# Optimization experiments

Measured on AMD Instinct MI355X. Metric: run time of the kernel, lower is better.

The kernel has to match this reference:

```python
import jax, jax.numpy as jnp
import numpy as np

B, S, D = 16, 1024, 384
H, DH = 6, 64  # head_dim = hidden // heads


def setup_inputs() -> dict:
    key = jax.random.key(0)
    ks = jax.random.split(key, 9)
    std = 0.02
    return {
        "x": jax.random.normal(ks[0], (B, S, D), jnp.float32),
        "Wq": jax.random.normal(ks[1], (H, D, DH), jnp.float32) * std,
        "bq": jax.random.normal(ks[2], (H, DH), jnp.float32) * std,
        "Wk": jax.random.normal(ks[3], (H, D, DH), jnp.float32) * std,
        "bk": jax.random.normal(ks[4], (H, DH), jnp.float32) * std,
        "Wv": jax.random.normal(ks[5], (H, D, DH), jnp.float32) * std,
        "bv": jax.random.normal(ks[6], (H, DH), jnp.float32) * std,
        "Wo": jax.random.normal(ks[7], (D, D), jnp.float32) * std,  # [out, in] like nn.Linear
        "bo": jax.random.normal(ks[8], (D,), jnp.float32) * std,
    }


def reference(x, Wq, bq, Wk, bk, Wv, bv, Wo, bo):
    # Per-head q/k/v projections (stacked over heads h)
    q = jnp.einsum("bsd,hde->bhse", x, Wq) + bq[None, :, None, :]
    k = jnp.einsum("bsd,hde->bhse", x, Wk) + bk[None, :, None, :]
    v = jnp.einsum("bsd,hde->bhse", x, Wv) + bv[None, :, None, :]
    # Explicit softmax attention (dropout prob = 0.0 in config)
    scores = jnp.einsum("bhse,bhte->bhst", q, k) / jnp.sqrt(jnp.float32(DH))
    probs = jax.nn.softmax(scores, axis=-1)
    ctx = jnp.einsum("bhst,bhte->bhse", probs, v)  # [B,H,S,DH]
    # Concat heads along last dim: [B,S,H*DH]
    concat = jnp.transpose(ctx, (0, 2, 1, 3)).reshape(B, S, H * DH)
    # Output projection (nn.Linear: y = x @ W^T + b)
    out = jnp.einsum("bsd,ed->bse", concat, Wo) + bo
    return out
```

## Files before the change

### kernel.cpp

```cpp
#include <hip/hip_runtime.h>
#include <hip/hip_bf16.h>

typedef __attribute__((ext_vector_type(8))) short short8;
typedef __attribute__((ext_vector_type(4))) short short4v;
typedef __attribute__((ext_vector_type(4))) float float4v;
typedef __attribute__((ext_vector_type(2))) float float2v;
typedef __attribute__((ext_vector_type(4))) int int4v;

#define MFMA16(a,b,c) __builtin_amdgcn_mfma_f32_16x16x32_bf16((a),(b),(c),0,0,0)
#define EXP2(x) __builtin_amdgcn_exp2f(x)

static constexpr int Bz = 16, Sq = 1024, Dm = 384, Hh = 6, Dh = 64;
static constexpr int Mtok = Bz * Sq;
static constexpr int NQKV = 1152;

__device__ __forceinline__ short f2bf(float f) {
  union { float f; unsigned u; } v; v.f = f;
  unsigned r = v.u + 0x7fffu + ((v.u >> 16) & 1u);
  return (short)(r >> 16);
}

__device__ __forceinline__ unsigned cvtpk(float a, float b) {
  unsigned d;
  asm("v_cvt_pk_bf16_f32 %0, %1, %2" : "=v"(d) : "v"(a), "v"(b));
  return d;
}

__device__ __forceinline__ void gload16(const void* src, void* lds) {
  __builtin_amdgcn_global_load_lds(
      (const __attribute__((address_space(1))) unsigned int*)src,
      (__attribute__((address_space(3))) unsigned int*)lds, 16, 0, 0);
}

__device__ __forceinline__ int vperm(int s) {
  return (s & ~31) | ((s & 12) << 1) | ((s & 16) >> 2) | (s & 3);
}

__global__ __launch_bounds__(256) void conv_x(const float* __restrict__ x,
                                              short* __restrict__ xb) {
  const int i = (blockIdx.x * 256 + threadIdx.x) * 8;
  float4v v0 = *(const float4v*)(x + i);
  float4v v1 = *(const float4v*)(x + i + 4);
  short8 o;
  o[0] = f2bf(v0[0]); o[1] = f2bf(v0[1]); o[2] = f2bf(v0[2]); o[3] = f2bf(v0[3]);
  o[4] = f2bf(v1[0]); o[5] = f2bf(v1[1]); o[6] = f2bf(v1[2]); o[7] = f2bf(v1[3]);
  *(short8*)(xb + i) = o;
}

__global__ __launch_bounds__(256) void conv_w(const float* __restrict__ Wq,
                                              const float* __restrict__ Wk,
                                              const float* __restrict__ Wv,
                                              const float* __restrict__ bq,
                                              const float* __restrict__ bk,
                                              const float* __restrict__ bv,
                                              const float* __restrict__ Wo,
                                              short* __restrict__ Wt,
                                              float* __restrict__ bias,
                                              short* __restrict__ Wob) {
  const float SCL = 0.125f * 1.44269504088896340736f;
  const int i = blockIdx.x * 256 + threadIdx.x;
  const int NW = NQKV * Dm;
  if (i < NW) {
    const int c = i / Dm, d = i % Dm;
    const int p = c / 384, rr = c % 384;
    const int h = rr >> 6, dh = rr & 63;
    const float* W = (p == 0) ? Wq : ((p == 1) ? Wk : Wv);
    float w = W[(h * Dm + d) * Dh + dh];
    if (p == 0) w *= SCL;
    Wt[c * Dm + d] = f2bf(w);
  } else if (i < NW + NQKV) {
    const int c = i - NW;
    const int p = c / 384, rr = c % 384;
    const int h = rr >> 6, dh = rr & 63;
    const float* bb = (p == 0) ? bq : ((p == 1) ? bk : bv);
    float b = bb[h * Dh + dh];
    if (p == 0) b *= SCL;
    bias[c] = b;
  } else if (i < NW + NQKV + Dm * Dm) {
    const int j = i - NW - NQKV;
    Wob[j] = f2bf(Wo[j]);
  }
}

__global__ __launch_bounds__(256) void qkv_gemm(const short* __restrict__ Xb,
                                                const short* __restrict__ Wt,
                                                const float* __restrict__ bias,
                                                short* __restrict__ qkv,
                                                short* __restrict__ vt) {
  __shared__ char smem[49152];
  const int tid = threadIdx.x;
  const int wave = tid >> 6, lane = tid & 63;
  const int r = lane & 15, g = lane >> 4;
  const int wr = wave >> 1, wc = wave & 1;

  const int flat = blockIdx.x;
  const int w = (flat & 7) * 144 + (flat >> 3);
  const int bx = w % 9, by = w / 9;
  const int bm0 = by * 128, bn0 = bx * 128;
  const int m0 = bm0 + wr * 64, n0 = bn0 + wc * 64;

  float bv_n[4];
#pragma unroll
  for (int ni = 0; ni < 4; ++ni) bv_n[ni] = bias[n0 + ni * 16 + r];
  asm volatile("s_waitcnt vmcnt(0)" ::: "memory");

  const char *aSrc0, *aSrc1, *bSrc0, *bSrc1;
  {
    const int o0 = tid * 16, o1 = 4096 + tid * 16;
    const int lr0 = o0 >> 7, cb0 = (o0 & 127) ^ ((lr0 & 7) << 4);
    const int lr1 = o1 >> 7, cb1 = (o1 & 127) ^ ((lr1 & 7) << 4);
    const int m_0 = 2 * lr0 + (cb0 >> 6), kb0 = cb0 & 63;
    const int m_1 = 2 * lr1 + (cb1 >> 6), kb1 = cb1 & 63;
    aSrc0 = (const char*)(Xb + (bm0 + m_0) * Dm) + kb0;
    aSrc1 = (const char*)(Xb + (bm0 + m_1) * Dm) + kb1;
    bSrc0 = (const char*)(Wt + (bn0 + m_0) * Dm) + kb0;
    bSrc1 = (const char*)(Wt + (bn0 + m_1) * Dm) + kb1;
  }
  auto stage = [&](int t, int buf) {
    char* base = smem + buf * 16384;
    const int kb = t * 64;
    gload16(aSrc0 + kb, base + wave * 1024);
    gload16(aSrc1 + kb, base + 4096 + wave * 1024);
    gload16(bSrc0 + kb, base + 8192 + wave * 1024);
    gload16(bSrc1 + kb, base + 12288 + wave * 1024);
  };

  int aOff[4], bOff[4];
#pragma unroll
  for (int i = 0; i < 4; ++i) {
    const int m = wr * 64 + i * 16 + r;
    const int lr = m >> 1;
    aOff[i] = lr * 128 + ((((m & 1) << 6) | (16 * g)) ^ ((lr & 7) << 4));
    const int n = wc * 64 + i * 16 + r;
    const int lrn = n >> 1;
    bOff[i] = 8192 + lrn * 128 + ((((n & 1) << 6) | (16 * g)) ^ ((lrn & 7) << 4));
  }

  float4v acc[4][4] = {};
  auto compute = [&](int buf) {
    const char* sb = smem + buf * 16384;
    short8 a[4], b[4];
#pragma unroll
    for (int i = 0; i < 4; ++i) a[i] = *(const short8*)(sb + aOff[i]);
#pragma unroll
    for (int i = 0; i < 4; ++i) b[i] = *(const short8*)(sb + bOff[i]);
#pragma unroll
    for (int mi = 0; mi < 4; ++mi)
#pragma unroll
      for (int ni = 0; ni < 4; ++ni)
        acc[mi][ni] = MFMA16(a[mi], b[ni], acc[mi][ni]);
  };

  stage(0, 0);
  stage(1, 1);
#pragma unroll 1
  for (int t = 0; t < 10; ++t) {
    asm volatile("s_waitcnt vmcnt(4)" ::: "memory");
    __builtin_amdgcn_s_barrier();
    compute(t % 3);
    stage(t + 2, (t + 2) % 3);
  }
  asm volatile("s_waitcnt vmcnt(4)" ::: "memory");
  __builtin_amdgcn_s_barrier();
  compute(1);
  asm volatile("s_waitcnt vmcnt(0)" ::: "memory");
  __builtin_amdgcn_s_barrier();
  compute(2);

#pragma unroll
  for (int ni = 0; ni < 4; ++ni) {
    const int col = n0 + ni * 16 + r;
    const int p = col / 384, rr2 = col % 384;
    const int h = rr2 >> 6, dh = rr2 & 63;
    const float bv = bv_n[ni];
#pragma unroll
    for (int mi = 0; mi < 4; ++mi) {
#pragma unroll
      for (int rp = 0; rp < 2; ++rp) {
        const unsigned u = cvtpk(acc[mi][ni][2 * rp] + bv,
                                 acc[mi][ni][2 * rp + 1] + bv);
        const int mg = m0 + mi * 16 + 4 * g + 2 * rp;
        if (p < 2) {
          qkv[mg * NQKV + col] = (short)u;
          qkv[(mg + 1) * NQKV + col] = (short)(u >> 16);
        } else {
          const int bb = mg >> 10, s = mg & 1023;
          const int sp = vperm(s);
          short* vp = vt + ((bb * Hh + h) * Dh + dh) * Sq;
          *(unsigned*)(vp + sp) = u;
        }
      }
    }
  }
}

__global__ __launch_bounds__(256) void attn(const short* __restrict__ qkv,
                                            const short* __restrict__ vt,
                                            short* __restrict__ ctx) {
  __shared__ char smem[49152];
  const int tid = threadIdx.x;
  const int wave = tid >> 6, lane = tid & 63;
  const int r = lane & 15, g = lane >> 4;
  const int xr = (r & 7) << 4;
  const int flat = blockIdx.x;
  const int w = (flat & 7) * 96 + (flat >> 3);
  const int qb = w & 7, bh = w >> 3;
  const int b = bh / Hh, h = bh % Hh;
  const int tok0 = b * Sq;
  const int qw = qb * 128 + wave * 32;

  short8 qf[2][2];
#pragma unroll
  for (int f = 0; f < 2; ++f) {
    const short* qp = qkv + (tok0 + qw + 16 * f + r) * NQKV + h * Dh;
    qf[f][0] = *(const short8*)(qp + 8 * g);
    qf[f][1] = *(const short8*)(qp + 32 + 8 * g);
  }
  asm volatile("s_waitcnt vmcnt(0)" ::: "memory");

  const short* kg = qkv + tok0 * NQKV + 384 + h * Dh;
  const short* vg = vt + (b * Hh + h) * Dh * Sq;

  const int o0 = wave * 2048 + lane * 16;
  const int row0 = o0 >> 7, cb0 = (o0 & 127) ^ ((row0 & 7) << 4);
  const int o1 = o0 + 1024;
  const int row1 = o1 >> 7, cb1 = (o1 & 127) ^ ((row1 & 7) << 4);

#define STAGE(T, BUFSEL)                                                        \
  {                                                                             \
    char* kb_ = smem + (BUFSEL) * 16384;                                        \
    const int kv_ = (T) * 64;                                                   \
    gload16((const char*)(kg + (kv_ + row0) * NQKV) + cb0, kb_ + wave * 2048);  \
    gload16((const char*)(vg + row0 * Sq + kv_) + cb0, kb_ + 8192 + wave * 2048);\
    gload16((const char*)(kg + (kv_ + row1) * NQKV) + cb1, kb_ + wave * 2048 + 1024);\
    gload16((const char*)(vg + row1 * Sq + kv_) + cb1, kb_ + 8192 + wave * 2048 + 1024);\
  }

  int kOff[4][2], vOff[4][2];
#pragma unroll
  for (int kt = 0; kt < 4; ++kt)
#pragma unroll
    for (int c = 0; c < 2; ++c)
      kOff[kt][c] = (16 * kt + r) * 128 + ((64 * c + 16 * g) ^ xr);
#pragma unroll
  for (int d = 0; d < 4; ++d)
#pragma unroll
    for (int h2 = 0; h2 < 2; ++h2)
      vOff[d][h2] = (16 * d + r) * 128 + ((64 * h2 + 16 * g) ^ xr);

  float4v acc[4][2] = {};
  float2v lsum2[2] = {};

  auto compute = [&](int bufsel) {
    const char* kb = smem + bufsel * 16384;
    const char* vb = kb + 8192;
    short8 kf[4][2];
#pragma unroll
    for (int kt = 0; kt < 4; ++kt) {
      kf[kt][0] = *(const short8*)(kb + kOff[kt][0]);
      kf[kt][1] = *(const short8*)(kb + kOff[kt][1]);
    }
    short8 vf[4][2];
#pragma unroll
    for (int d = 0; d < 4; ++d)
#pragma unroll
      for (int h2 = 0; h2 < 2; ++h2)
        vf[d][h2] = *(const short8*)(vb + vOff[d][h2]);
    float4v s[4][2];
    __builtin_amdgcn_s_setprio(1);
#pragma unroll
    for (int kt = 0; kt < 4; ++kt)
#pragma unroll
      for (int f = 0; f < 2; ++f) {
        float4v z = {};
        z = MFMA16(kf[kt][0], qf[f][0], z);
        z = MFMA16(kf[kt][1], qf[f][1], z);
        s[kt][f] = z;
      }
    __builtin_amdgcn_s_setprio(0);
    short8 pa[2][2];
#pragma unroll
    for (int f = 0; f < 2; ++f) {
      float2v ps2 = {};
#pragma unroll
      for (int h2 = 0; h2 < 2; ++h2) {
        float e0[4], e1[4];
#pragma unroll
        for (int j = 0; j < 4; ++j) {
          e0[j] = EXP2(s[2 * h2][f][j]);
          e1[j] = EXP2(s[2 * h2 + 1][f][j]);
        }
#pragma unroll
        for (int j = 0; j < 2; ++j) {
          float2v p0 = {e0[2 * j], e0[2 * j + 1]};
          float2v p1 = {e1[2 * j], e1[2 * j + 1]};
          ps2 += p0 + p1;
        }
        int4v wv;
        wv[0] = (int)cvtpk(e0[0], e0[1]);
        wv[1] = (int)cvtpk(e0[2], e0[3]);
        wv[2] = (int)cvtpk(e1[0], e1[1]);
        wv[3] = (int)cvtpk(e1[2], e1[3]);
        pa[f][h2] = __builtin_bit_cast(short8, wv);
      }
      lsum2[f] += ps2;
    }
    __builtin_amdgcn_s_setprio(1);
#pragma unroll
    for (int d = 0; d < 4; ++d)
#pragma unroll
      for (int f = 0; f < 2; ++f) {
        acc[d][f] = MFMA16(pa[f][0], vf[d][0], acc[d][f]);
        acc[d][f] = MFMA16(pa[f][1], vf[d][1], acc[d][f]);
      }
    __builtin_amdgcn_s_setprio(0);
  };

  STAGE(0, 0)
  STAGE(1, 1)
#pragma unroll 1
  for (int t = 0; t < 14; ++t) {
    asm volatile("s_waitcnt vmcnt(4)" ::: "memory");
    __builtin_amdgcn_s_barrier();
    compute(t % 3);
    STAGE(t + 2, (t + 2) % 3)
  }
  asm volatile("s_waitcnt vmcnt(4)" ::: "memory");
  __builtin_amdgcn_s_barrier();
  compute(2);
  asm volatile("s_waitcnt vmcnt(0)" ::: "memory");
  __builtin_amdgcn_s_barrier();
  compute(0);

#pragma unroll
  for (int f = 0; f < 2; ++f) {
    float lsum = lsum2[f][0] + lsum2[f][1];
    lsum += __shfl_xor(lsum, 16);
    lsum += __shfl_xor(lsum, 32);
    float il[4];
#pragma unroll
    for (int reg = 0; reg < 4; ++reg) il[reg] = 1.f / __shfl(lsum, 4 * g + reg);
#pragma unroll
    for (int d = 0; d < 4; ++d) {
      short* cp = ctx + (tok0 + qw + 16 * f + 4 * g) * Dm + h * Dh + 16 * d + r;
#pragma unroll
      for (int reg = 0; reg < 4; ++reg)
        cp[reg * Dm] = f2bf(acc[d][f][reg] * il[reg]);
    }
  }
}

__global__ __launch_bounds__(256) void out_gemm(const short* __restrict__ ctx,
                                                const short* __restrict__ Wob,
                                                const float* __restrict__ bo,
                                                float* __restrict__ out) {
  __shared__ char smem[49152];
  const int tid = threadIdx.x;
  const int wave = tid >> 6, lane = tid & 63;
  const int r = lane & 15, g = lane >> 4;
  const int wr = wave >> 1, wc = wave & 1;

  const int flat = blockIdx.x;
  const int w = (flat & 7) * 48 + (flat >> 3);
  const int bx = w % 3, by = w / 3;
  const int bm0 = by * 128, bn0 = bx * 128;
  const int m0 = bm0 + wr * 64, n0 = bn0 + wc * 64;

  float bv_n[4];
#pragma unroll
  for (int ni = 0; ni < 4; ++ni) bv_n[ni] = bo[n0 + ni * 16 + r];
  asm volatile("s_waitcnt vmcnt(0)" ::: "memory");

  const char *aSrc0, *aSrc1, *bSrc0, *bSrc1;
  {
    const int o0 = tid * 16, o1 = 4096 + tid * 16;
    const int lr0 = o0 >> 7, cb0 = (o0 & 127) ^ ((lr0 & 7) << 4);
    const int lr1 = o1 >> 7, cb1 = (o1 & 127) ^ ((lr1 & 7) << 4);
    const int m_0 = 2 * lr0 + (cb0 >> 6), kb0 = cb0 & 63;
    const int m_1 = 2 * lr1 + (cb1 >> 6), kb1 = cb1 & 63;
    aSrc0 = (const char*)(ctx + (bm0 + m_0) * Dm) + kb0;
    aSrc1 = (const char*)(ctx + (bm0 + m_1) * Dm) + kb1;
    bSrc0 = (const char*)(Wob + (bn0 + m_0) * Dm) + kb0;
    bSrc1 = (const char*)(Wob + (bn0 + m_1) * Dm) + kb1;
  }
  auto stage = [&](int t, int buf) {
    char* base = smem + buf * 16384;
    const int kb = t * 64;
    gload16(aSrc0 + kb, base + wave * 1024);
    gload16(aSrc1 + kb, base + 4096 + wave * 1024);
    gload16(bSrc0 + kb, base + 8192 + wave * 1024);
    gload16(bSrc1 + kb, base + 12288 + wave * 1024);
  };

  int aOff[4], bOff[4];
#pragma unroll
  for (int i = 0; i < 4; ++i) {
    const int m = wr * 64 + i * 16 + r;
    const int lr = m >> 1;
    aOff[i] = lr * 128 + ((((m & 1) << 6) | (16 * g)) ^ ((lr & 7) << 4));
    const int n = wc * 64 + i * 16 + r;
    const int lrn = n >> 1;
    bOff[i] = 8192 + lrn * 128 + ((((n & 1) << 6) | (16 * g)) ^ ((lrn & 7) << 4));
  }

  float4v acc[4][4] = {};
  auto compute = [&](int buf) {
    const char* sb = smem + buf * 16384;
    short8 a[4], b[4];
#pragma unroll
    for (int i = 0; i < 4; ++i) a[i] = *(const short8*)(sb + aOff[i]);
#pragma unroll
    for (int i = 0; i < 4; ++i) b[i] = *(const short8*)(sb + bOff[i]);
#pragma unroll
    for (int mi = 0; mi < 4; ++mi)
#pragma unroll
      for (int ni = 0; ni < 4; ++ni)
        acc[mi][ni] = MFMA16(a[mi], b[ni], acc[mi][ni]);
  };

  stage(0, 0);
  stage(1, 1);
#pragma unroll 1
  for (int t = 0; t < 10; ++t) {
    asm volatile("s_waitcnt vmcnt(4)" ::: "memory");
    __builtin_amdgcn_s_barrier();
    compute(t % 3);
    stage(t + 2, (t + 2) % 3);
  }
  asm volatile("s_waitcnt vmcnt(4)" ::: "memory");
  __builtin_amdgcn_s_barrier();
  compute(1);
  asm volatile("s_waitcnt vmcnt(0)" ::: "memory");
  __builtin_amdgcn_s_barrier();
  compute(2);

#pragma unroll
  for (int ni = 0; ni < 4; ++ni) {
    const int col = n0 + ni * 16 + r;
    const float bv = bv_n[ni];
#pragma unroll
    for (int mi = 0; mi < 4; ++mi) {
#pragma unroll
      for (int reg = 0; reg < 4; ++reg) {
        const int mg = m0 + mi * 16 + 4 * g + reg;
        out[mg * Dm + col] = acc[mi][ni][reg] + bv;
      }
    }
  }
}

extern "C" void kernel_launch(void* const* d_in, const int* in_sizes, int n_in,
                              void* d_out, int out_size, void* d_ws, size_t ws_size,
                              hipStream_t stream) {
  const float* x  = (const float*)d_in[0];
  const float* Wq = (const float*)d_in[1];
  const float* bq = (const float*)d_in[2];
  const float* Wk = (const float*)d_in[3];
  const float* bk = (const float*)d_in[4];
  const float* Wv = (const float*)d_in[5];
  const float* bv = (const float*)d_in[6];
  const float* Wo = (const float*)d_in[7];
  const float* bo = (const float*)d_in[8];
  float* out = (float*)d_out;

  char* ws = (char*)d_ws;
  short* Xb   = (short*)(ws);
  short* Wt   = (short*)(ws + 12582912);
  float* bias = (float*)(ws + 13467648);
  short* Wob  = (short*)(ws + 13472256);
  short* qkv  = (short*)(ws + 13767168);
  short* vt   = (short*)(ws + 51515904);
  short* ctx  = (short*)(ws + 64098816);

  conv_x<<<Mtok * Dm / (256 * 8), 256, 0, stream>>>(x, Xb);
  conv_w<<<(NQKV * Dm + NQKV + Dm * Dm + 255) / 256, 256, 0, stream>>>(
      Wq, Wk, Wv, bq, bk, bv, Wo, Wt, bias, Wob);
  qkv_gemm<<<1152, 256, 0, stream>>>(Xb, Wt, bias, qkv, vt);
  attn<<<768, 256, 0, stream>>>(qkv, vt, ctx);
  out_gemm<<<384, 256, 0, stream>>>(ctx, Wob, bo, out);
}
```

Baseline: 98.33 us.

## Software-pipeline QK^T with softmax·V in attention and merge conversion kernels

The attention inner loop is restructured so the QK^T MFMAs for the current KV tile are issued before the exp/softmax and PV MFMAs of the previous tile. This lets transcendental and MFMA work from adjacent tiles overlap. Scores and V fragments are carried across iterations in registers, which raises register pressure and may lower occupancy. Separately, the x and weight conversion kernels are fused into one prep launch to save a kernel launch.

```diff
diff --git a/kernel.cpp b/kernel.cpp
--- a/kernel.cpp
+++ b/kernel.cpp
@@ -36,30 +36,33 @@
   return (s & ~31) | ((s & 12) << 1) | ((s & 16) >> 2) | (s & 3);
 }
 
-__global__ __launch_bounds__(256) void conv_x(const float* __restrict__ x,
-                                              short* __restrict__ xb) {
-  const int i = (blockIdx.x * 256 + threadIdx.x) * 8;
-  float4v v0 = *(const float4v*)(x + i);
-  float4v v1 = *(const float4v*)(x + i + 4);
-  short8 o;
-  o[0] = f2bf(v0[0]); o[1] = f2bf(v0[1]); o[2] = f2bf(v0[2]); o[3] = f2bf(v0[3]);
-  o[4] = f2bf(v1[0]); o[5] = f2bf(v1[1]); o[6] = f2bf(v1[2]); o[7] = f2bf(v1[3]);
-  *(short8*)(xb + i) = o;
-}
-
-__global__ __launch_bounds__(256) void conv_w(const float* __restrict__ Wq,
-                                              const float* __restrict__ Wk,
-                                              const float* __restrict__ Wv,
-                                              const float* __restrict__ bq,
-                                              const float* __restrict__ bk,
-                                              const float* __restrict__ bv,
-                                              const float* __restrict__ Wo,
-                                              short* __restrict__ Wt,
-                                              float* __restrict__ bias,
-                                              short* __restrict__ Wob) {
+__global__ __launch_bounds__(256) void prep(const float* __restrict__ x,
+                                            const float* __restrict__ Wq,
+                                            const float* __restrict__ Wk,
+                                            const float* __restrict__ Wv,
+                                            const float* __restrict__ bq,
+                                            const float* __restrict__ bk,
+                                            const float* __restrict__ bv,
+                                            const float* __restrict__ Wo,
+                                            short* __restrict__ xb,
+                                            short* __restrict__ Wt,
+                                            float* __restrict__ bias,
+                                            short* __restrict__ Wob) {
   const float SCL = 0.125f * 1.44269504088896340736f;
-  const int i = blockIdx.x * 256 + threadIdx.x;
+  const int NX = Mtok * Dm / 8;
   const int NW = NQKV * Dm;
+  const int idx = blockIdx.x * 256 + threadIdx.x;
+  if (idx < NX) {
+    const int i = idx * 8;
+    float4v v0 = *(const float4v*)(x + i);
+    float4v v1 = *(const float4v*)(x + i + 4);
+    short8 o;
+    o[0] = f2bf(v0[0]); o[1] = f2bf(v0[1]); o[2] = f2bf(v0[2]); o[3] = f2bf(v0[3]);
+    o[4] = f2bf(v1[0]); o[5] = f2bf(v1[1]); o[6] = f2bf(v1[2]); o[7] = f2bf(v1[3]);
+    *(short8*)(xb + i) = o;
+    return;
+  }
+  const int i = idx - NX;
   if (i < NW) {
     const int c = i / Dm, d = i % Dm;
     const int p = c / 384, rr = c % 384;
@@ -250,23 +253,25 @@
 
   float4v acc[4][2] = {};
   float2v lsum2[2] = {};
-
-  auto compute = [&](int bufsel) {
+  float4v sP[4][2];
+  short8 vfP[4][2];
+
+  auto loadKV = [&](int bufsel, short8 (&kf)[4][2], short8 (&vf)[4][2]) {
     const char* kb = smem + bufsel * 16384;
     const char* vb = kb + 8192;
-    short8 kf[4][2];
 #pragma unroll
     for (int kt = 0; kt < 4; ++kt) {
       kf[kt][0] = *(const short8*)(kb + kOff[kt][0]);
       kf[kt][1] = *(const short8*)(kb + kOff[kt][1]);
     }
-    short8 vf[4][2];
 #pragma unroll
     for (int d = 0; d < 4; ++d)
 #pragma unroll
       for (int h2 = 0; h2 < 2; ++h2)
         vf[d][h2] = *(const short8*)(vb + vOff[d][h2]);
-    float4v s[4][2];
+  };
+
+  auto qkt = [&](const short8 (&kf)[4][2], float4v (&sD)[4][2]) {
     __builtin_amdgcn_s_setprio(1);
 #pragma unroll
     for (int kt = 0; kt < 4; ++kt)
@@ -275,9 +280,12 @@
         float4v z = {};
         z = MFMA16(kf[kt][0], qf[f][0], z);
         z = MFMA16(kf[kt][1], qf[f][1], z);
-        s[kt][f] = z;
+        sD[kt][f] = z;
       }
     __builtin_amdgcn_s_setprio(0);
+  };
+
+  auto softpv = [&]() {
     short8 pa[2][2];
 #pragma unroll
     for (int f = 0; f < 2; ++f) {
@@ -287,8 +295,8 @@
         float e0[4], e1[4];
 #pragma unroll
         for (int j = 0; j < 4; ++j) {
-          e0[j] = EXP2(s[2 * h2][f][j]);
-          e1[j] = EXP2(s[2 * h2 + 1][f][j]);
+          e0[j] = EXP2(sP[2 * h2][f][j]);
+          e1[j] = EXP2(sP[2 * h2 + 1][f][j]);
         }
 #pragma unroll
         for (int j = 0; j < 2; ++j) {
@@ -310,27 +318,47 @@
     for (int d = 0; d < 4; ++d)
 #pragma unroll
       for (int f = 0; f < 2; ++f) {
-        acc[d][f] = MFMA16(pa[f][0], vf[d][0], acc[d][f]);
-        acc[d][f] = MFMA16(pa[f][1], vf[d][1], acc[d][f]);
+        acc[d][f] = MFMA16(pa[f][0], vfP[d][0], acc[d][f]);
+        acc[d][f] = MFMA16(pa[f][1], vfP[d][1], acc[d][f]);
       }
     __builtin_amdgcn_s_setprio(0);
   };
 
   STAGE(0, 0)
   STAGE(1, 1)
-#pragma unroll 1
-  for (int t = 0; t < 14; ++t) {
-    asm volatile("s_waitcnt vmcnt(4)" ::: "memory");
-    __builtin_amdgcn_s_barrier();
-    compute(t % 3);
-    STAGE(t + 2, (t + 2) % 3)
-  }
   asm volatile("s_waitcnt vmcnt(4)" ::: "memory");
   __builtin_amdgcn_s_barrier();
-  compute(2);
-  asm volatile("s_waitcnt vmcnt(0)" ::: "memory");
-  __builtin_amdgcn_s_barrier();
-  compute(0);
+  {
+    short8 kf[4][2];
+    loadKV(0, kf, vfP);
+    qkt(kf, sP);
+  }
+  STAGE(2, 2)
+
+#pragma unroll 1
+  for (int t = 1; t <= 15; ++t) {
+    if (t < 15) {
+      asm volatile("s_waitcnt vmcnt(4)" ::: "memory");
+    } else {
+      asm volatile("s_waitcnt vmcnt(0)" ::: "memory");
+    }
+    __builtin_amdgcn_s_barrier();
+    short8 kf[4][2], vfC[4][2];
+    loadKV(t % 3, kf, vfC);
+    float4v sC[4][2];
+    qkt(kf, sC);
+    softpv();
+#pragma unroll
+    for (int kt = 0; kt < 4; ++kt)
+#pragma unroll
+      for (int f = 0; f < 2; ++f) sP[kt][f] = sC[kt][f];
+#pragma unroll
+    for (int d = 0; d < 4; ++d)
+#pragma unroll
+      for (int h2 = 0; h2 < 2; ++h2) vfP[d][h2] = vfC[d][h2];
+    if (t <= 13) STAGE(t + 2, (t + 2) % 3)
+  }
+  softpv();
 
 #pragma unroll
   for (int f = 0; f < 2; ++f) {
@@ -472,9 +500,9 @@
   short* vt   = (short*)(ws + 51515904);
   short* ctx  = (short*)(ws + 64098816);
 
-  conv_x<<<Mtok * Dm / (256 * 8), 256, 0, stream>>>(x, Xb);
-  conv_w<<<(NQKV * Dm + NQKV + Dm * Dm + 255) / 256, 256, 0, stream>>>(
-      Wq, Wk, Wv, bq, bk, bv, Wo, Wt, bias, Wob);
+  const int prepN = Mtok * Dm / 8 + NQKV * Dm + NQKV + Dm * Dm;
+  prep<<<(prepN + 255) / 256, 256, 0, stream>>>(x, Wq, Wk, Wv, bq, bk, bv, Wo,
+                                                Xb, Wt, bias, Wob);
   qkv_gemm<<<1152, 256, 0, stream>>>(Xb, Wt, bias, qkv, vt);
   attn<<<768, 256, 0, stream>>>(qkv, vt, ctx);
   out_gemm<<<384, 256, 0, stream>>>(ctx, Wob, bo, out);
```

Result: faster. 94.58 us, median of 2 (-3.8%).

## Halve attention waves with 64 query rows each, pipeline QK^T and softmax-PV, fuse prep kernels

Applied to the files above, without the earlier changes.

Each attention block now runs 2 waves instead of 4, and each wave handles 64 query rows. The point is to reuse every K/V fragment read from LDS across twice as many MFMAs. The per-tile compute is software-pipelined so the QK^T MFMAs for the next 16-row group are issued before softmax and PV of the current group. The staging loop issues 8 global-to-LDS loads per thread, and the waitcnt values are adjusted to match. The x conversion and weight conversion kernels are merged into one prep launch. The cost is higher register pressure and fewer waves per CU for hiding latency.

```diff
diff --git a/kernel.cpp b/kernel.cpp
--- a/kernel.cpp
+++ b/kernel.cpp
@@ -36,30 +36,33 @@
   return (s & ~31) | ((s & 12) << 1) | ((s & 16) >> 2) | (s & 3);
 }
 
-__global__ __launch_bounds__(256) void conv_x(const float* __restrict__ x,
-                                              short* __restrict__ xb) {
-  const int i = (blockIdx.x * 256 + threadIdx.x) * 8;
-  float4v v0 = *(const float4v*)(x + i);
-  float4v v1 = *(const float4v*)(x + i + 4);
-  short8 o;
-  o[0] = f2bf(v0[0]); o[1] = f2bf(v0[1]); o[2] = f2bf(v0[2]); o[3] = f2bf(v0[3]);
-  o[4] = f2bf(v1[0]); o[5] = f2bf(v1[1]); o[6] = f2bf(v1[2]); o[7] = f2bf(v1[3]);
-  *(short8*)(xb + i) = o;
-}
-
-__global__ __launch_bounds__(256) void conv_w(const float* __restrict__ Wq,
-                                              const float* __restrict__ Wk,
-                                              const float* __restrict__ Wv,
-                                              const float* __restrict__ bq,
-                                              const float* __restrict__ bk,
-                                              const float* __restrict__ bv,
-                                              const float* __restrict__ Wo,
-                                              short* __restrict__ Wt,
-                                              float* __restrict__ bias,
-                                              short* __restrict__ Wob) {
+__global__ __launch_bounds__(256) void prep(const float* __restrict__ x,
+                                            const float* __restrict__ Wq,
+                                            const float* __restrict__ Wk,
+                                            const float* __restrict__ Wv,
+                                            const float* __restrict__ bq,
+                                            const float* __restrict__ bk,
+                                            const float* __restrict__ bv,
+                                            const float* __restrict__ Wo,
+                                            short* __restrict__ xb,
+                                            short* __restrict__ Wt,
+                                            float* __restrict__ bias,
+                                            short* __restrict__ Wob) {
   const float SCL = 0.125f * 1.44269504088896340736f;
-  const int i = blockIdx.x * 256 + threadIdx.x;
+  const int NX = Mtok * Dm / 8;
   const int NW = NQKV * Dm;
+  const int idx = blockIdx.x * 256 + threadIdx.x;
+  if (idx < NX) {
+    const int i = idx * 8;
+    float4v v0 = *(const float4v*)(x + i);
+    float4v v1 = *(const float4v*)(x + i + 4);
+    short8 o;
+    o[0] = f2bf(v0[0]); o[1] = f2bf(v0[1]); o[2] = f2bf(v0[2]); o[3] = f2bf(v0[3]);
+    o[4] = f2bf(v1[0]); o[5] = f2bf(v1[1]); o[6] = f2bf(v1[2]); o[7] = f2bf(v1[3]);
+    *(short8*)(xb + i) = o;
+    return;
+  }
+  const int i = idx - NX;
   if (i < NW) {
     const int c = i / Dm, d = i % Dm;
     const int p = c / 384, rr = c % 384;
@@ -194,7 +197,7 @@
   }
 }
 
-__global__ __launch_bounds__(256) void attn(const short* __restrict__ qkv,
+__global__ __launch_bounds__(128) void attn(const short* __restrict__ qkv,
                                             const short* __restrict__ vt,
                                             short* __restrict__ ctx) {
   __shared__ char smem[49152];
@@ -207,11 +210,11 @@
   const int qb = w & 7, bh = w >> 3;
   const int b = bh / Hh, h = bh % Hh;
   const int tok0 = b * Sq;
-  const int qw = qb * 128 + wave * 32;
-
-  short8 qf[2][2];
-#pragma unroll
-  for (int f = 0; f < 2; ++f) {
+  const int qw = qb * 128 + wave * 64;
+
+  short8 qf[4][2];
+#pragma unroll
+  for (int f = 0; f < 4; ++f) {
     const short* qp = qkv + (tok0 + qw + 16 * f + r) * NQKV + h * Dh;
     qf[f][0] = *(const short8*)(qp + 8 * g);
     qf[f][1] = *(const short8*)(qp + 32 + 8 * g);
@@ -221,19 +224,25 @@
   const short* kg = qkv + tok0 * NQKV + 384 + h * Dh;
   const short* vg = vt + (b * Hh + h) * Dh * Sq;
 
-  const int o0 = wave * 2048 + lane * 16;
-  const int row0 = o0 >> 7, cb0 = (o0 & 127) ^ ((row0 & 7) << 4);
-  const int o1 = o0 + 1024;
-  const int row1 = o1 >> 7, cb1 = (o1 & 127) ^ ((row1 & 7) << 4);
+  int rowj[4], cbj[4];
+#pragma unroll
+  for (int j = 0; j < 4; ++j) {
+    const int o = j * 2048 + wave * 1024 + lane * 16;
+    rowj[j] = o >> 7;
+    cbj[j] = (o & 127) ^ ((rowj[j] & 7) << 4);
+  }
 
 #define STAGE(T, BUFSEL)                                                        \
   {                                                                             \
     char* kb_ = smem + (BUFSEL) * 16384;                                        \
     const int kv_ = (T) * 64;                                                   \
-    gload16((const char*)(kg + (kv_ + row0) * NQKV) + cb0, kb_ + wave * 2048);  \
-    gload16((const char*)(vg + row0 * Sq + kv_) + cb0, kb_ + 8192 + wave * 2048);\
-    gload16((const char*)(kg + (kv_ + row1) * NQKV) + cb1, kb_ + wave * 2048 + 1024);\
-    gload16((const char*)(vg + row1 * Sq + kv_) + cb1, kb_ + 8192 + wave * 2048 + 1024);\
+    _Pragma("unroll")                                                           \
+    for (int j = 0; j < 4; ++j) {                                               \
+      gload16((const char*)(kg + (kv_ + rowj[j]) * NQKV) + cbj[j],              \
+              kb_ + j * 2048 + wave * 1024);                                    \
+      gload16((const char*)(vg + rowj[j] * Sq + kv_) + cbj[j],                  \
+              kb_ + 8192 + j * 2048 + wave * 1024);                             \
+    }                                                                           \
   }
 
   int kOff[4][2], vOff[4][2];
@@ -248,84 +257,92 @@
     for (int h2 = 0; h2 < 2; ++h2)
       vOff[d][h2] = (16 * d + r) * 128 + ((64 * h2 + 16 * g) ^ xr);
 
-  float4v acc[4][2] = {};
-  float2v lsum2[2] = {};
-
-  auto compute = [&](int bufsel) {
+  float4v acc[4][4] = {};
+  float2v lsum2[4] = {};
+  short8 kf[4][2], vf[4][2];
+
+  auto loadKV = [&](int bufsel) {
     const char* kb = smem + bufsel * 16384;
     const char* vb = kb + 8192;
-    short8 kf[4][2];
 #pragma unroll
     for (int kt = 0; kt < 4; ++kt) {
       kf[kt][0] = *(const short8*)(kb + kOff[kt][0]);
       kf[kt][1] = *(const short8*)(kb + kOff[kt][1]);
     }
-    short8 vf[4][2];
 #pragma unroll
     for (int d = 0; d < 4; ++d)
 #pragma unroll
       for (int h2 = 0; h2 < 2; ++h2)
         vf[d][h2] = *(const short8*)(vb + vOff[d][h2]);
-    float4v s[4][2];
+  };
+
+  auto qkt_f = [&](int f, float4v (&sD)[4]) {
     __builtin_amdgcn_s_setprio(1);
 #pragma unroll
-    for (int kt = 0; kt < 4; ++kt)
-#pragma unroll
-      for (int f = 0; f < 2; ++f) {
-        float4v z = {};
-        z = MFMA16(kf[kt][0], qf[f][0], z);
-        z = MFMA16(kf[kt][1], qf[f][1], z);
-        s[kt][f] = z;
+    for (int kt = 0; kt < 4; ++kt) {
+      float4v z = {};
+      z = MFMA16(kf[kt][0], qf[f][0], z);
+      z = MFMA16(kf[kt][1], qf[f][1], z);
+      sD[kt] = z;
+    }
+    __builtin_amdgcn_s_setprio(0);
+  };
+
+  auto softpv_f = [&](int f, const float4v (&sIn)[4]) {
+    short8 pa[2];
+    float2v ps2 = {};
+#pragma unroll
+    for (int h2 = 0; h2 < 2; ++h2) {
+      float e0[4], e1[4];
+#pragma unroll
+      for (int j = 0; j < 4; ++j) {
+        e0[j] = EXP2(sIn[2 * h2][j]);
+        e1[j] = EXP2(sIn[2 * h2 + 1][j]);
       }
+#pragma unroll
+      for (int j = 0; j < 2; ++j) {
+        float2v p0 = {e0[2 * j], e0[2 * j + 1]};
+        float2v p1 = {e1[2 * j], e1[2 * j + 1]};
+        ps2 += p0 + p1;
+      }
+      int4v wv;
+      wv[0] = (int)cvtpk(e0[0], e0[1]);
+      wv[1] = (int)cvtpk(e0[2], e0[3]);
+      wv[2] = (int)cvtpk(e1[0], e1[1]);
+      wv[3] = (int)cvtpk(e1[2], e1[3]);
+      pa[h2] = __builtin_bit_cast(short8, wv);
+    }
+    lsum2[f] += ps2;
+    __builtin_amdgcn_s_setprio(1);
+#pragma unroll
+    for (int d = 0; d < 4; ++d) {
+      acc[d][f] = MFMA16(pa[0], vf[d][0], acc[d][f]);
+      acc[d][f] = MFMA16(pa[1], vf[d][1], acc[d][f]);
+    }
     __builtin_amdgcn_s_setprio(0);
-    short8 pa[2][2];
-#pragma unroll
-    for (int f = 0; f < 2; ++f) {
-      float2v ps2 = {};
-#pragma unroll
-      for (int h2 = 0; h2 < 2; ++h2) {
-        float e0[4], e1[4];
-#pragma unroll
-        for (int j = 0; j < 4; ++j) {
-          e0[j] = EXP2(s[2 * h2][f][j]);
-          e1[j] = EXP2(s[2 * h2 + 1][f][j]);
-        }
-#pragma unroll
-        for (int j = 0; j < 2; ++j) {
-          float2v p0 = {e0[2 * j], e0[2 * j + 1]};
-          float2v p1 = {e1[2 * j], e1[2 * j + 1]};
-          ps2 += p0 + p1;
-        }
-        int4v wv;
-        wv[0] = (int)cvtpk(e0[0], e0[1]);
-        wv[1] = (int)cvtpk(e0[2], e0[3]);
-        wv[2] = (int)cvtpk(e1[0], e1[1]);
-        wv[3] = (int)cvtpk(e1[2], e1[3]);
-        pa[f][h2] = __builtin_bit_cast(short8, wv);
-      }
-      lsum2[f] += ps2;
-    }
-    __builtin_amdgcn_s_setprio(1);
-#pragma unroll
-    for (int d = 0; d < 4; ++d)
-#pragma unroll
-      for (int f = 0; f < 2; ++f) {
-        acc[d][f] = MFMA16(pa[f][0], vf[d][0], acc[d][f]);
-        acc[d][f] = MFMA16(pa[f][1], vf[d][1], acc[d][f]);
-      }
-    __builtin_amdgcn_s_setprio(0);
+  };
+
+  auto compute = [&](int bufsel) {
+    loadKV(bufsel);
+    float4v s2[2][4];
+    qkt_f(0, s2[0]);
+#pragma unroll
+    for (int f = 0; f < 4; ++f) {
+      if (f < 3) qkt_f(f + 1, s2[(f + 1) & 1]);
+      softpv_f(f, s2[f & 1]);
+    }
   };
 
   STAGE(0, 0)
   STAGE(1, 1)
 #pragma unroll 1
   for (int t = 0; t < 14; ++t) {
-    asm volatile("s_waitcnt vmcnt(4)" ::: "memory");
+    asm volatile("s_waitcnt vmcnt(8)" ::: "memory");
     __builtin_amdgcn_s_barrier();
     compute(t % 3);
     STAGE(t + 2, (t + 2) % 3)
   }
-  asm volatile("s_waitcnt vmcnt(4)" ::: "memory");
+  asm volatile("s_waitcnt vmcnt(8)" ::: "memory");
   __builtin_amdgcn_s_barrier();
   compute(2);
   asm volatile("s_waitcnt vmcnt(0)" ::: "memory");
@@ -333,7 +350,7 @@
   compute(0);
 
 #pragma unroll
-  for (int f = 0; f < 2; ++f) {
+  for (int f = 0; f < 4; ++f) {
     float lsum = lsum2[f][0] + lsum2[f][1];
     lsum += __shfl_xor(lsum, 16);
     lsum += __shfl_xor(lsum, 32);
@@ -472,10 +489,10 @@
   short* vt   = (short*)(ws + 51515904);
   short* ctx  = (short*)(ws + 64098816);
 
-  conv_x<<<Mtok * Dm / (256 * 8), 256, 0, stream>>>(x, Xb);
-  conv_w<<<(NQKV * Dm + NQKV + Dm * Dm + 255) / 256, 256, 0, stream>>>(
-      Wq, Wk, Wv, bq, bk, bv, Wo, Wt, bias, Wob);
+  const int prepN = Mtok * Dm / 8 + NQKV * Dm + NQKV + Dm * Dm;
+  prep<<<(prepN + 255) / 256, 256, 0, stream>>>(x, Wq, Wk, Wv, bq, bk, bv, Wo,
+                                                Xb, Wt, bias, Wob);
   qkv_gemm<<<1152, 256, 0, stream>>>(Xb, Wt, bias, qkv, vt);
-  attn<<<768, 256, 0, stream>>>(qkv, vt, ctx);
+  attn<<<768, 128, 0, stream>>>(qkv, vt, ctx);
   out_gemm<<<384, 256, 0, stream>>>(ctx, Wob, bo, out);
 }
```

Result: slower. 109.1 us (+10.9%).
